# Optimization experiments

Measured on AMD Instinct MI355X. Metric: run time of the kernel, lower is better.

## Reference

```python
import jax, jax.numpy as jnp
import numpy as np

B, S, D, H, KS, VS, O = 4, 2048, 1024, 16, 64, 64, 1024


def setup_inputs() -> dict:
    key = jax.random.key(0)
    ks = jax.random.split(key, 11)
    def w(k, shp):
        return jax.random.normal(k, shp, dtype=jnp.float32) * 0.02
    return {
        "Q": jax.random.normal(ks[0], (B, S, D), dtype=jnp.float32),
        "K": jax.random.normal(ks[1], (B, S, D), dtype=jnp.float32),
        "V": jax.random.normal(ks[2], (B, S, D), dtype=jnp.float32),
        # per-head projection weights stacked over heads (equivalent to 3*H separate nn.Linear)
        "Wq": w(ks[3], (H, D, KS)), "bq": w(ks[4], (H, KS)),
        "Wk": w(ks[5], (H, D, KS)), "bk": w(ks[6], (H, KS)),
        "Wv": w(ks[7], (H, D, VS)), "bv": w(ks[8], (H, VS)),
        "Wo": w(ks[9], (H * VS, O)), "bo": w(ks[10], (O,)),
    }


def reference(Q, K, V, Wq, bq, Wk, bk, Wv, bv, Wo, bo):
    scale = jnp.sqrt(jnp.asarray(KS, dtype=Q.dtype))
    # per-head linear projections (vectorized over heads)
    q = jnp.einsum('bsd,hdk->bhsk', Q, Wq) + bq[:, None, :]   # [B,H,S,KS]
    k = jnp.einsum('bsd,hdk->bhsk', K, Wk) + bk[:, None, :]   # [B,H,S,KS]
    v = jnp.einsum('bsd,hdv->bhsv', V, Wv) + bv[:, None, :]   # [B,H,S,VS]
    # scaled dot-product attention, full S x S scores per head
    scores = jnp.einsum('bhsk,bhtk->bhst', q, k) / scale       # [B,H,S,S]
    attn = jax.nn.softmax(scores, axis=-1)
    heads = jnp.einsum('bhst,bhtv->bhsv', attn, v)             # [B,H,S,VS]
    # concat heads along feature dim -> [B,S,H*VS]
    cat = jnp.transpose(heads, (0, 2, 1, 3)).reshape(B, S, H * VS)
    return cat @ Wo + bo
```

## Files before the change

kernel.cpp:

```cpp
#include <hip/hip_runtime.h>
#include <hip/hip_fp16.h>
#include <cstdint>
#include <cstddef>

typedef _Float16 f16;
typedef _Float16 f16x8 __attribute__((ext_vector_type(8)));
typedef _Float16 f16x4 __attribute__((ext_vector_type(4)));
typedef float    f32x4 __attribute__((ext_vector_type(4)));

#define MFMA(a, b, c) __builtin_amdgcn_mfma_f32_16x16x32_f16(a, b, c, 0, 0, 0)


__device__ __forceinline__ void gload_lds16(const f16* g, f16* l) {
    __builtin_amdgcn_global_load_lds(
        (const __attribute__((address_space(1))) void*)g,
        (__attribute__((address_space(3))) void*)l, 16, 0, 0);
}

__global__ void k_convert3(const float* __restrict__ Q, const float* __restrict__ K,
                           const float* __restrict__ V, f16* __restrict__ Qh,
                           f16* __restrict__ Kh, f16* __restrict__ Vh) {
    const int seg = blockIdx.x >> 11;
    const int lb  = blockIdx.x & 2047;
    const float* src = seg == 0 ? Q : (seg == 1 ? K : V);
    f16* dst = seg == 0 ? Qh : (seg == 1 ? Kh : Vh);
    int i = lb * blockDim.x + threadIdx.x;
    for (; i < 2097152; i += 524288) {
        float4 v = ((const float4*)src)[i];
        f16x4 h;
        h[0] = (f16)v.x; h[1] = (f16)v.y; h[2] = (f16)v.z; h[3] = (f16)v.w;
        ((f16x4*)dst)[i] = h;
    }
}

__global__ void k_transpose_all(const float* __restrict__ Wq, const float* __restrict__ Wk,
                                const float* __restrict__ Wv, const float* __restrict__ Wo,
                                f16* __restrict__ WT, f16* __restrict__ WoT) {
    __shared__ float T[64][65];
    const int bx = blockIdx.x;
    const int widx = bx >> 8, sub = bx & 255;
    const int nb = sub >> 4, db = sub & 15;
    const int tid = threadIdx.x;
    const float* W = widx == 0 ? Wq : (widx == 1 ? Wk : (widx == 2 ? Wv : Wo));
    f16* Wt = (widx < 3) ? (WT + (size_t)widx * 1048576) : WoT;
    const float* src = (widx < 3) ? (W + nb * 65536 + db * 4096)
                                  : (W + db * 65536 + nb * 64);
    const int rstride = (widx < 3) ? 64 : 1024;
    {
        int nn = tid & 63, d0 = tid >> 6;
#pragma unroll
        for (int p = 0; p < 16; ++p) {
            int dd = p * 4 + d0;
            T[dd][nn] = src[dd * rstride + nn];
        }
    }
    __syncthreads();
    {
        int dd = tid & 63, n0 = tid >> 6;
#pragma unroll
        for (int p = 0; p < 16; ++p) {
            int nn = p * 4 + n0;
            Wt[(size_t)(nb * 64 + nn) * 1024 + db * 64 + dd] = (f16)T[dd][nn];
        }
    }
}

__global__ __launch_bounds__(256) void k_gemm_qkv(
    const f16* __restrict__ Qh, const f16* __restrict__ Kh, const f16* __restrict__ Vh,
    const f16* __restrict__ WT, const float* __restrict__ bq,
    const float* __restrict__ bk, const float* __restrict__ bv,
    f16* __restrict__ qout, f16* __restrict__ kout, f16* __restrict__ vout, float SC) {
    __shared__ f16 As[128 * 32];
    __shared__ f16 Bs[128 * 32];
    const int yy = blockIdx.y;
    const int seg = yy >> 3;
    const f16* A    = seg == 0 ? Qh : (seg == 1 ? Kh : Vh);
    const f16* Bt   = WT + (size_t)seg * 1048576;
    const float* bias = seg == 0 ? bq : (seg == 1 ? bk : bv);
    const float scale = seg == 0 ? SC : 1.0f;

    const int tid = threadIdx.x;
    const int wid = tid >> 6, lane = tid & 63;
    const int wr = wid >> 1, wc = wid & 1;
    const int lr = lane & 15, lg = lane >> 4;
    const int row0 = blockIdx.x * 128, col0 = (yy & 7) * 128;

    f32x4 acc[4][4];
#pragma unroll
    for (int m = 0; m < 4; ++m)
#pragma unroll
        for (int n = 0; n < 4; ++n) acc[m][n] = (f32x4){0.f, 0.f, 0.f, 0.f};

    const int c0 = tid, c1 = tid + 256;
    const int r0 = c0 >> 2, cb0 = (c0 & 3) * 8;
    const int r1 = c1 >> 2, cb1 = (c1 & 3) * 8;

    for (int k0 = 0; k0 < 1024; k0 += 32) {
        __syncthreads();
        gload_lds16(&A[(size_t)(row0 + r0) * 1024 + k0 + cb0], &As[c0 * 8]);
        gload_lds16(&Bt[(size_t)(col0 + r0) * 1024 + k0 + cb0], &Bs[c0 * 8]);
        gload_lds16(&A[(size_t)(row0 + r1) * 1024 + k0 + cb1], &As[c1 * 8]);
        gload_lds16(&Bt[(size_t)(col0 + r1) * 1024 + k0 + cb1], &Bs[c1 * 8]);
        __syncthreads();
        f16x8 af[4], bf[4];
#pragma unroll
        for (int m = 0; m < 4; ++m) af[m] = *(const f16x8*)&As[(wr * 64 + m * 16 + lr) * 32 + lg * 8];
#pragma unroll
        for (int n = 0; n < 4; ++n) bf[n] = *(const f16x8*)&Bs[(wc * 64 + n * 16 + lr) * 32 + lg * 8];
#pragma unroll
        for (int m = 0; m < 4; ++m)
#pragma unroll
            for (int n = 0; n < 4; ++n) acc[m][n] = MFMA(af[m], bf[n], acc[m][n]);
    }

#pragma unroll
    for (int m = 0; m < 4; ++m) {
#pragma unroll
        for (int n = 0; n < 4; ++n) {
            int col = col0 + wc * 64 + n * 16 + lr;
            float bv_ = bias[col];
            int rowb = row0 + wr * 64 + m * 16 + lg * 4;
            int srow = rowb & 2047;
            if (seg == 0) {
#pragma unroll
                for (int r = 0; r < 4; ++r) {
                    int row = rowb + r;
                    size_t a = ((size_t)((row >> 11) * 16 + (col >> 6)) * 2048 + (row & 2047)) * 64 + (col & 63);
                    qout[a] = (f16)((acc[m][n][r] + bv_) * scale);
                }
            } else if (seg == 1) {
                int ks5 = srow & 31;
                int p0 = ((ks5 >> 2) & 1) * 16 + (ks5 >> 3) * 4 + (ks5 & 3);
                size_t abase = (size_t)((rowb >> 11) * 16 + (col >> 6)) * 131072
                             + (size_t)(srow >> 5) * 2048
                             + (size_t)(p0 >> 4) * 512
                             + (size_t)((col & 63) >> 5) * 1024
                             + (size_t)((col & 31) >> 3) * 128
                             + (col & 7);
#pragma unroll
                for (int r = 0; r < 4; ++r)
                    kout[abase + (size_t)((p0 & 15) + r) * 8] = (f16)(acc[m][n][r] + bv_);
            } else {
                size_t a = (size_t)((rowb >> 11) * 16 + (col >> 6)) * 131072
                         + (size_t)(srow >> 5) * 2048
                         + (size_t)((col & 63) >> 4) * 512
                         + (size_t)((srow & 31) >> 3) * 128
                         + (size_t)(col & 15) * 8
                         + (srow & 7);
                f16x4 ov;
#pragma unroll
                for (int r = 0; r < 4; ++r) ov[r] = (f16)(acc[m][n][r] + bv_);
                *(f16x4*)&vout[a] = ov;
            }
        }
    }
}

__global__ __launch_bounds__(256) void k_gemm_out(const f16* __restrict__ A,
                                                  const f16* __restrict__ Bt,
                                                  const float* __restrict__ bias,
                                                  float* __restrict__ Cout) {
    __shared__ f16 As[128 * 32];
    __shared__ f16 Bs[128 * 32];
    const int tid = threadIdx.x;
    const int wid = tid >> 6, lane = tid & 63;
    const int wr = wid >> 1, wc = wid & 1;
    const int lr = lane & 15, lg = lane >> 4;
    const int row0 = blockIdx.x * 128, col0 = blockIdx.y * 128;

    f32x4 acc[4][4];
#pragma unroll
    for (int m = 0; m < 4; ++m)
#pragma unroll
        for (int n = 0; n < 4; ++n) acc[m][n] = (f32x4){0.f, 0.f, 0.f, 0.f};

    const int c0 = tid, c1 = tid + 256;
    const int r0 = c0 >> 2, cb0 = (c0 & 3) * 8;
    const int r1 = c1 >> 2, cb1 = (c1 & 3) * 8;

    for (int k0 = 0; k0 < 1024; k0 += 32) {
        __syncthreads();
        gload_lds16(&A[(size_t)(row0 + r0) * 1024 + k0 + cb0], &As[c0 * 8]);
        gload_lds16(&Bt[(size_t)(col0 + r0) * 1024 + k0 + cb0], &Bs[c0 * 8]);
        gload_lds16(&A[(size_t)(row0 + r1) * 1024 + k0 + cb1], &As[c1 * 8]);
        gload_lds16(&Bt[(size_t)(col0 + r1) * 1024 + k0 + cb1], &Bs[c1 * 8]);
        __syncthreads();
        f16x8 af[4], bf[4];
#pragma unroll
        for (int m = 0; m < 4; ++m) af[m] = *(const f16x8*)&As[(wr * 64 + m * 16 + lr) * 32 + lg * 8];
#pragma unroll
        for (int n = 0; n < 4; ++n) bf[n] = *(const f16x8*)&Bs[(wc * 64 + n * 16 + lr) * 32 + lg * 8];
#pragma unroll
        for (int m = 0; m < 4; ++m)
#pragma unroll
            for (int n = 0; n < 4; ++n) acc[m][n] = MFMA(af[m], bf[n], acc[m][n]);
    }

#pragma unroll
    for (int m = 0; m < 4; ++m) {
#pragma unroll
        for (int n = 0; n < 4; ++n) {
            int col = col0 + wc * 64 + n * 16 + lr;
            float bv = bias[col];
#pragma unroll
            for (int r = 0; r < 4; ++r) {
                int row = row0 + wr * 64 + m * 16 + lg * 4 + r;
                Cout[(size_t)row * 1024 + col] = acc[m][n][r] + bv;
            }
        }
    }
}

__global__ __launch_bounds__(256, 4) void k_attn(const f16* __restrict__ q,
                                                 const f16* __restrict__ k2,
                                                 const f16* __restrict__ v2,
                                                 f16* __restrict__ cat) {
    const int g = blockIdx.x;
    const int xcd = g & 7, i = g >> 3;
    const int bh = xcd * 8 + (i >> 4);
    const int qb = i & 15;
    const int b = bh >> 4, h = bh & 15;

    const int tid = threadIdx.x, wid = tid >> 6, lane = tid & 63;
    const int lr = lane & 15, lg = lane >> 4;
    const int qw = qb * 128 + wid * 32;

    __shared__ f16 Ks[2][2048];
    __shared__ f16 Vs[2][2048];

    const float THR = 8.0f;

    f16x8 qf[2][2];
#pragma unroll
    for (int qt = 0; qt < 2; ++qt)
#pragma unroll
        for (int hf = 0; hf < 2; ++hf)
            qf[qt][hf] = *(const f16x8*)&q[((size_t)bh * 2048 + qw + qt * 16 + lr) * 64 + hf * 32 + lg * 8];

    const f16* kt = k2 + (size_t)bh * 131072;
    const f16* vt = v2 + (size_t)bh * 131072;
    const int so = tid * 8;
    const int fo = lane * 8;

    f32x4 o[2][4];
#pragma unroll
    for (int qt = 0; qt < 2; ++qt)
#pragma unroll
        for (int m = 0; m < 4; ++m) o[qt][m] = (f32x4){0.f, 0.f, 0.f, 0.f};
    float m_r[2] = {0.f, 0.f}, l_p[2] = {0.f, 0.f};

    gload_lds16(kt + so, &Ks[0][so]);
    gload_lds16(vt + so, &Vs[0][so]);
    __syncthreads();

    for (int tt = 0; tt < 64; ++tt) {
        const f16* Kc = &Ks[tt & 1][0];
        const f16* Vc = &Vs[tt & 1][0];
        gload_lds16(kt + (tt + 1) * 2048 + so, &Ks[(tt & 1) ^ 1][so]);
        gload_lds16(vt + (tt + 1) * 2048 + so, &Vs[(tt & 1) ^ 1][so]);

        f16x8 ka0 = *(const f16x8*)&Kc[fo];
        f16x8 ka1 = *(const f16x8*)&Kc[fo + 1024];
        f16x8 ka2 = *(const f16x8*)&Kc[fo + 512];
        f16x8 ka3 = *(const f16x8*)&Kc[fo + 1536];

        f32x4 st[2][2];
        __builtin_amdgcn_s_setprio(1);
#pragma unroll
        for (int qt = 0; qt < 2; ++qt) {
            float nm = -m_r[qt];
            f32x4 z = (f32x4){nm, nm, nm, nm};
            z = MFMA(ka0, qf[qt][0], z);
            z = MFMA(ka1, qf[qt][1], z);
            st[qt][0] = z;
            f32x4 z2 = (f32x4){nm, nm, nm, nm};
            z2 = MFMA(ka2, qf[qt][0], z2);
            z2 = MFMA(ka3, qf[qt][1], z2);
            st[qt][1] = z2;
        }
        __builtin_amdgcn_s_setprio(0);

        f16x8 vv0 = *(const f16x8*)&Vc[fo];
        f16x8 vv1 = *(const f16x8*)&Vc[fo + 512];
        f16x8 vv2 = *(const f16x8*)&Vc[fo + 1024];
        f16x8 vv3 = *(const f16x8*)&Vc[fo + 1536];

        {
            float lm[2];
#pragma unroll
            for (int qt = 0; qt < 2; ++qt) {
                float a0 = fmaxf(fmaxf(st[qt][0][0], st[qt][0][1]), st[qt][0][2]);
                float b0 = fmaxf(fmaxf(st[qt][0][3], st[qt][1][0]), st[qt][1][1]);
                float c0 = fmaxf(fmaxf(st[qt][1][2], st[qt][1][3]), a0);
                lm[qt] = fmaxf(b0, c0);
            }
            if (__any((lm[0] > THR) || (lm[1] > THR))) {
#pragma unroll
                for (int qt = 0; qt < 2; ++qt) {
                    float t0 = lm[qt];
                    t0 = fmaxf(t0, __shfl_xor(t0, 16, 64));
                    t0 = fmaxf(t0, __shfl_xor(t0, 32, 64));
                    float delta = fmaxf(0.f, t0);
                    float alpha = __builtin_amdgcn_exp2f(-delta);
#pragma unroll
                    for (int m = 0; m < 4; ++m)
#pragma unroll
                        for (int r = 0; r < 4; ++r) o[qt][m][r] *= alpha;
                    l_p[qt] *= alpha;
                    m_r[qt] += delta;
#pragma unroll
                    for (int t = 0; t < 2; ++t)
#pragma unroll
                        for (int r = 0; r < 4; ++r) st[qt][t][r] -= delta;
                }
            }
        }

        f16x8 pf[2];
#pragma unroll
        for (int qt = 0; qt < 2; ++qt) {
            float ps = 0.f;
            union { uint32_t u[4]; f16x8 v; } bb;
#pragma unroll
            for (int t = 0; t < 2; ++t)
#pragma unroll
                for (int pr = 0; pr < 2; ++pr) {
                    float e0 = __builtin_amdgcn_exp2f(st[qt][t][2 * pr]);
                    float e1 = __builtin_amdgcn_exp2f(st[qt][t][2 * pr + 1]);
                    ps += e0 + e1;
                    auto hp = __builtin_amdgcn_cvt_pkrtz(e0, e1);
                    bb.u[t * 2 + pr] = __builtin_bit_cast(uint32_t, hp);
                }
            l_p[qt] += ps;
            pf[qt] = bb.v;
        }

        __builtin_amdgcn_s_setprio(1);
#pragma unroll
        for (int qt = 0; qt < 2; ++qt) {
            o[qt][0] = MFMA(vv0, pf[qt], o[qt][0]);
            o[qt][1] = MFMA(vv1, pf[qt], o[qt][1]);
            o[qt][2] = MFMA(vv2, pf[qt], o[qt][2]);
            o[qt][3] = MFMA(vv3, pf[qt], o[qt][3]);
        }
        __builtin_amdgcn_s_setprio(0);

        __syncthreads();
    }

#pragma unroll
    for (int qt = 0; qt < 2; ++qt) {
        float l = l_p[qt];
        l += __shfl_xor(l, 16, 64);
        l += __shfl_xor(l, 32, 64);
        float inv = 1.f / l;
        size_t cb = ((size_t)b * 2048 + qw + qt * 16 + lr) * 1024 + h * 64 + lg * 4;
#pragma unroll
        for (int m = 0; m < 4; ++m) {
            f16x4 ov;
#pragma unroll
            for (int r = 0; r < 4; ++r) ov[r] = (f16)(o[qt][m][r] * inv);
            *(f16x4*)&cat[cb + m * 16] = ov;
        }
    }
}

extern "C" void kernel_launch(void* const* d_in, const int* in_sizes, int n_in,
                              void* d_out, int out_size, void* d_ws, size_t ws_size,
                              hipStream_t stream) {
    const float* Q  = (const float*)d_in[0];
    const float* K  = (const float*)d_in[1];
    const float* V  = (const float*)d_in[2];
    const float* Wq = (const float*)d_in[3];
    const float* bq = (const float*)d_in[4];
    const float* Wk = (const float*)d_in[5];
    const float* bk = (const float*)d_in[6];
    const float* Wv = (const float*)d_in[7];
    const float* bv = (const float*)d_in[8];
    const float* Wo = (const float*)d_in[9];
    const float* bo = (const float*)d_in[10];

    char* ws = (char*)d_ws;
    size_t off = 0;
    auto alloc = [&](size_t bytes) {
        char* p = ws + off;
        off += (bytes + 255) & ~(size_t)255;
        return p;
    };
    f16* Qh  = (f16*)alloc(8192ULL * 1024 * 2);
    f16* Kh  = (f16*)alloc(8192ULL * 1024 * 2);
    f16* Vh  = (f16*)alloc(8192ULL * 1024 * 2);
    f16* WT  = (f16*)alloc(3ULL * 1024 * 1024 * 2);
    f16* WoT = (f16*)alloc(1024ULL * 1024 * 2);
    f16* qb  = (f16*)alloc(8192ULL * 1024 * 2);
    f16* kb2 = (f16*)alloc(8192ULL * 1024 * 2);
    f16* vb2 = (f16*)alloc(8192ULL * 1024 * 2);
    f16* cat = (f16*)alloc(8192ULL * 1024 * 2);

    k_convert3<<<6144, 256, 0, stream>>>(Q, K, V, Qh, Kh, Vh);
    k_transpose_all<<<1024, 256, 0, stream>>>(Wq, Wk, Wv, Wo, WT, WoT);

    const float SC = 0.125f * 1.44269504089f;
    k_gemm_qkv<<<dim3(64, 24), 256, 0, stream>>>(Qh, Kh, Vh, WT, bq, bk, bv,
                                                 qb, kb2, vb2, SC);

    k_attn<<<1024, 256, 0, stream>>>(qb, kb2, vb2, cat);

    k_gemm_out<<<dim3(64, 8), 256, 0, stream>>>(cat, WoT, bo, (float*)d_out);
}
```

Baseline: 211.3 us.

## Process two KV tiles per barrier with four-stage LDS ring buffer

The attention inner loop now handles two 32-key tiles between barriers and keeps a 4-slot LDS ring for K and V, prefetching the next two tiles while computing the current pair. This halves the number of __syncthreads calls and gives async global-to-LDS loads more time to land. LDS use per block doubles, which may reduce occupancy. The s_setprio hints around the MFMA groups are dropped. The last iteration prefetches past the end of the per-head K/V buffers, as the old loop also did.

Measured after the change: 211.9 us (median of 2 runs). About the same (+0.3%).

```diff
diff --git a/kernel.cpp b/kernel.cpp
--- a/kernel.cpp
+++ b/kernel.cpp
@@ -211,6 +211,86 @@
     }
 }
 
+#define ATTN_TILE(Kc, Vc)                                                     \
+    do {                                                                      \
+        f16x8 ka0 = *(const f16x8*)&(Kc)[fo];                                 \
+        f16x8 ka1 = *(const f16x8*)&(Kc)[fo + 1024];                          \
+        f16x8 ka2 = *(const f16x8*)&(Kc)[fo + 512];                           \
+        f16x8 ka3 = *(const f16x8*)&(Kc)[fo + 1536];                          \
+        f32x4 st[2][2];                                                       \
+        _Pragma("unroll")                                                     \
+        for (int qt = 0; qt < 2; ++qt) {                                      \
+            float nm = -m_r[qt];                                              \
+            f32x4 z = (f32x4){nm, nm, nm, nm};                                \
+            z = MFMA(ka0, qf[qt][0], z);                                      \
+            z = MFMA(ka1, qf[qt][1], z);                                      \
+            st[qt][0] = z;                                                    \
+            f32x4 z2 = (f32x4){nm, nm, nm, nm};                               \
+            z2 = MFMA(ka2, qf[qt][0], z2);                                    \
+            z2 = MFMA(ka3, qf[qt][1], z2);                                    \
+            st[qt][1] = z2;                                                   \
+        }                                                                     \
+        f16x8 vv0 = *(const f16x8*)&(Vc)[fo];                                 \
+        f16x8 vv1 = *(const f16x8*)&(Vc)[fo + 512];                           \
+        f16x8 vv2 = *(const f16x8*)&(Vc)[fo + 1024];                          \
+        f16x8 vv3 = *(const f16x8*)&(Vc)[fo + 1536];                          \
+        {                                                                     \
+            float lm[2];                                                      \
+            _Pragma("unroll")                                                 \
+            for (int qt = 0; qt < 2; ++qt) {                                  \
+                float a0 = fmaxf(fmaxf(st[qt][0][0], st[qt][0][1]), st[qt][0][2]); \
+                float b0 = fmaxf(fmaxf(st[qt][0][3], st[qt][1][0]), st[qt][1][1]); \
+                float c0 = fmaxf(fmaxf(st[qt][1][2], st[qt][1][3]), a0);      \
+                lm[qt] = fmaxf(b0, c0);                                       \
+            }                                                                 \
+            if (__any((lm[0] > THR) || (lm[1] > THR))) {                      \
+                _Pragma("unroll")                                             \
+                for (int qt = 0; qt < 2; ++qt) {                              \
+                    float t0 = lm[qt];                                        \
+                    t0 = fmaxf(t0, __shfl_xor(t0, 16, 64));                   \
+                    t0 = fmaxf(t0, __shfl_xor(t0, 32, 64));                   \
+                    float delta = fmaxf(0.f, t0);                             \
+                    float alpha = __builtin_amdgcn_exp2f(-delta);             \
+                    _Pragma("unroll")                                         \
+                    for (int m = 0; m < 4; ++m)                               \
+                        _Pragma("unroll")                                     \
+                        for (int r = 0; r < 4; ++r) o[qt][m][r] *= alpha;     \
+                    l_p[qt] *= alpha;                                         \
+                    m_r[qt] += delta;                                         \
+                    _Pragma("unroll")                                         \
+                    for (int t = 0; t < 2; ++t)                               \
+                        _Pragma("unroll")                                     \
+                        for (int r = 0; r < 4; ++r) st[qt][t][r] -= delta;    \
+                }                                                             \
+            }                                                                 \
+        }                                                                     \
+        f16x8 pf[2];                                                          \
+        _Pragma("unroll")                                                     \
+        for (int qt = 0; qt < 2; ++qt) {                                      \
+            float ps = 0.f;                                                   \
+            union { uint32_t u[4]; f16x8 v; } bb;                             \
+            _Pragma("unroll")                                                 \
+            for (int t = 0; t < 2; ++t)                                       \
+                _Pragma("unroll")                                             \
+                for (int pr = 0; pr < 2; ++pr) {                              \
+                    float e0 = __builtin_amdgcn_exp2f(st[qt][t][2 * pr]);     \
+                    float e1 = __builtin_amdgcn_exp2f(st[qt][t][2 * pr + 1]); \
+                    ps += e0 + e1;                                            \
+                    auto hp = __builtin_amdgcn_cvt_pkrtz(e0, e1);             \
+                    bb.u[t * 2 + pr] = __builtin_bit_cast(uint32_t, hp);      \
+                }                                                             \
+            l_p[qt] += ps;                                                    \
+            pf[qt] = bb.v;                                                    \
+        }                                                                     \
+        _Pragma("unroll")                                                     \
+        for (int qt = 0; qt < 2; ++qt) {                                      \
+            o[qt][0] = MFMA(vv0, pf[qt], o[qt][0]);                           \
+            o[qt][1] = MFMA(vv1, pf[qt], o[qt][1]);                           \
+            o[qt][2] = MFMA(vv2, pf[qt], o[qt][2]);                           \
+            o[qt][3] = MFMA(vv3, pf[qt], o[qt][3]);                           \
+        }                                                                     \
+    } while (0)
+
 __global__ __launch_bounds__(256, 4) void k_attn(const f16* __restrict__ q,
                                                  const f16* __restrict__ k2,
                                                  const f16* __restrict__ v2,
@@ -225,8 +305,8 @@
     const int lr = lane & 15, lg = lane >> 4;
     const int qw = qb * 128 + wid * 32;
 
-    __shared__ f16 Ks[2][2048];
-    __shared__ f16 Vs[2][2048];
+    __shared__ f16 Ks[4][2048];
+    __shared__ f16 Vs[4][2048];
 
     const float THR = 8.0f;
 
@@ -251,99 +331,22 @@
 
     gload_lds16(kt + so, &Ks[0][so]);
     gload_lds16(vt + so, &Vs[0][so]);
+    gload_lds16(kt + 2048 + so, &Ks[1][so]);
+    gload_lds16(vt + 2048 + so, &Vs[1][so]);
     __syncthreads();
 
-    for (int tt = 0; tt < 64; ++tt) {
-        const f16* Kc = &Ks[tt & 1][0];
-        const f16* Vc = &Vs[tt & 1][0];
-        gload_lds16(kt + (tt + 1) * 2048 + so, &Ks[(tt & 1) ^ 1][so]);
-        gload_lds16(vt + (tt + 1) * 2048 + so, &Vs[(tt & 1) ^ 1][so]);
-
-        f16x8 ka0 = *(const f16x8*)&Kc[fo];
-        f16x8 ka1 = *(const f16x8*)&Kc[fo + 1024];
-        f16x8 ka2 = *(const f16x8*)&Kc[fo + 512];
-        f16x8 ka3 = *(const f16x8*)&Kc[fo + 1536];
-
-        f32x4 st[2][2];
-        __builtin_amdgcn_s_setprio(1);
-#pragma unroll
-        for (int qt = 0; qt < 2; ++qt) {
-            float nm = -m_r[qt];
-            f32x4 z = (f32x4){nm, nm, nm, nm};
-            z = MFMA(ka0, qf[qt][0], z);
-            z = MFMA(ka1, qf[qt][1], z);
-            st[qt][0] = z;
-            f32x4 z2 = (f32x4){nm, nm, nm, nm};
-            z2 = MFMA(ka2, qf[qt][0], z2);
-            z2 = MFMA(ka3, qf[qt][1], z2);
-            st[qt][1] = z2;
-        }
-        __builtin_amdgcn_s_setprio(0);
-
-        f16x8 vv0 = *(const f16x8*)&Vc[fo];
-        f16x8 vv1 = *(const f16x8*)&Vc[fo + 512];
-        f16x8 vv2 = *(const f16x8*)&Vc[fo + 1024];
-        f16x8 vv3 = *(const f16x8*)&Vc[fo + 1536];
-
-        {
-            float lm[2];
-#pragma unroll
-            for (int qt = 0; qt < 2; ++qt) {
-                float a0 = fmaxf(fmaxf(st[qt][0][0], st[qt][0][1]), st[qt][0][2]);
-                float b0 = fmaxf(fmaxf(st[qt][0][3], st[qt][1][0]), st[qt][1][1]);
-                float c0 = fmaxf(fmaxf(st[qt][1][2], st[qt][1][3]), a0);
-                lm[qt] = fmaxf(b0, c0);
-            }
-            if (__any((lm[0] > THR) || (lm[1] > THR))) {
-#pragma unroll
-                for (int qt = 0; qt < 2; ++qt) {
-                    float t0 = lm[qt];
-                    t0 = fmaxf(t0, __shfl_xor(t0, 16, 64));
-                    t0 = fmaxf(t0, __shfl_xor(t0, 32, 64));
-                    float delta = fmaxf(0.f, t0);
-                    float alpha = __builtin_amdgcn_exp2f(-delta);
-#pragma unroll
-                    for (int m = 0; m < 4; ++m)
-#pragma unroll
-                        for (int r = 0; r < 4; ++r) o[qt][m][r] *= alpha;
-                    l_p[qt] *= alpha;
-                    m_r[qt] += delta;
-#pragma unroll
-                    for (int t = 0; t < 2; ++t)
-#pragma unroll
-                        for (int r = 0; r < 4; ++r) st[qt][t][r] -= delta;
-                }
-            }
-        }
-
-        f16x8 pf[2];
-#pragma unroll
-        for (int qt = 0; qt < 2; ++qt) {
-            float ps = 0.f;
-            union { uint32_t u[4]; f16x8 v; } bb;
-#pragma unroll
-            for (int t = 0; t < 2; ++t)
-#pragma unroll
-                for (int pr = 0; pr < 2; ++pr) {
-                    float e0 = __builtin_amdgcn_exp2f(st[qt][t][2 * pr]);
-                    float e1 = __builtin_amdgcn_exp2f(st[qt][t][2 * pr + 1]);
-                    ps += e0 + e1;
-                    auto hp = __builtin_amdgcn_cvt_pkrtz(e0, e1);
-                    bb.u[t * 2 + pr] = __builtin_bit_cast(uint32_t, hp);
-                }
-            l_p[qt] += ps;
-            pf[qt] = bb.v;
-        }
-
-        __builtin_amdgcn_s_setprio(1);
-#pragma unroll
-        for (int qt = 0; qt < 2; ++qt) {
-            o[qt][0] = MFMA(vv0, pf[qt], o[qt][0]);
-            o[qt][1] = MFMA(vv1, pf[qt], o[qt][1]);
-            o[qt][2] = MFMA(vv2, pf[qt], o[qt][2]);
-            o[qt][3] = MFMA(vv3, pf[qt], o[qt][3]);
-        }
-        __builtin_amdgcn_s_setprio(0);
+    for (int pp = 0; pp < 32; ++pp) {
+        const int t0 = 2 * pp;
+        const int ba = t0 & 3, bb2 = (t0 + 1) & 3;
+        const int bc = (t0 + 2) & 3, bd = (t0 + 3) & 3;
+
+        gload_lds16(kt + (size_t)(t0 + 2) * 2048 + so, &Ks[bc][so]);
+        gload_lds16(vt + (size_t)(t0 + 2) * 2048 + so, &Vs[bc][so]);
+        gload_lds16(kt + (size_t)(t0 + 3) * 2048 + so, &Ks[bd][so]);
+        gload_lds16(vt + (size_t)(t0 + 3) * 2048 + so, &Vs[bd][so]);
+
+        ATTN_TILE(&Ks[ba][0], &Vs[ba][0]);
+        ATTN_TILE(&Ks[bb2][0], &Vs[bb2][0]);
 
         __syncthreads();
     }
```
